# Kernel optimization log

Hardware: AMD Instinct MI355X
Metric: run time of the kernel (lower is better)

The kernel has to match this reference:

```python
import jax, jax.numpy as jnp
import numpy as np


def setup_inputs() -> dict:
    key = jax.random.key(0)
    B, F, H, W, C_out = 8, 64, 128, 128, 32
    V = H * W                     # grid vertices
    E = 3 * V                     # edges; flattened connectivity has 6V entries -> degree 6
    F2 = F // 2
    dim_channel = 6 * F2          # 192
    mid = dim_channel // 2        # 96
    out_ch = 2 * C_out            # 64
    k1, k2, k3, k4 = jax.random.split(key, 4)
    features = jax.random.normal(k1, (B, F, E), dtype=jnp.float32)
    # each vertex appears exactly 6 times in the flattened connectivity
    conn_flat = jax.random.permutation(k2, jnp.tile(jnp.arange(V, dtype=jnp.int32), 6))
    connectivity = conn_flat.reshape(E, 2)
    W1 = jax.random.normal(k3, (dim_channel, mid), dtype=jnp.float32) / np.sqrt(dim_channel)
    b1 = jnp.zeros((mid,), dtype=jnp.float32)
    W2 = jax.random.normal(k4, (mid, out_ch), dtype=jnp.float32) / np.sqrt(mid)
    b2 = jnp.zeros((out_ch,), dtype=jnp.float32)
    return {"features": features, "connectivity": connectivity,
            "output_dim": (H, W, C_out), "W1": W1, "b1": b1, "W2": W2, "b2": b2}


def _occurrence_rank(edges):
    # occ[i] = number of j < i with edges[j] == edges[i] (matches the serial
    # images_index bookkeeping in the torch loop). Stable argsort groups equal
    # vertices while preserving original order within a group.
    n = edges.shape[0]
    order = jnp.argsort(edges)            # stable by default in jax
    sorted_e = edges[order]
    first = jnp.searchsorted(sorted_e, sorted_e, side='left')
    rank_sorted = (jnp.arange(n) - first).astype(jnp.int32)
    return jnp.zeros(n, dtype=jnp.int32).at[order].set(rank_sorted)


def reference(features, connectivity, output_dim, W1, b1, W2, b2):
    B, F, E = features.shape
    H, Wd, C_out = int(output_dim[0]), int(output_dim[1]), int(output_dim[2])
    V = H * Wd
    F2 = F // 2
    edges = connectivity.reshape(-1)                      # [2E]
    # [B, F, E] -> [B, E, F] -> [B, 2E, F/2]: one half-feature per edge endpoint
    mesh = jnp.transpose(features, (0, 2, 1)).reshape(B, 2 * E, F2)
    occ = _occurrence_rank(edges)                         # slot per endpoint, 0..5
    # scatter half-features into [B, V, 6, F/2]; (vertex, slot) pairs are unique
    img = jnp.zeros((B, V, 6, F2), features.dtype).at[:, edges, occ, :].set(mesh)
    x = img.reshape(B, H, Wd, 6 * F2).transpose(0, 3, 1, 2)   # [B, 6*F/2, H, W]
    # 1x1 ConvTranspose2d == pointwise GEMM (torch weight layout [in, out, 1, 1])
    y = jax.nn.relu(jnp.einsum('bihw,io->bohw', x, W1) + b1[None, :, None, None])
    out = jax.nn.relu(jnp.einsum('bihw,io->bohw', y, W2) + b2[None, :, None, None])
    return out
```

## Files before the change

kernel.cpp:

```cpp
#include <hip/hip_runtime.h>
#include <hip/hip_bf16.h>
#include <stdint.h>

namespace {
constexpr int Bb   = 8;
constexpr int Ff   = 64;
constexpr int Ee   = 49152;
constexpr int Vv   = 16384;
constexpr int F2   = 32;
constexpr int TWOE = 2 * Ee;
constexpr int MID  = 96;
constexpr int OUTC = 64;
constexpr int DIMC = 192;
}

typedef __attribute__((ext_vector_type(8))) short bf16x8;
typedef __attribute__((ext_vector_type(4))) float f32x4;

__global__ void zero_cnt(int* __restrict__ cnt) {
    int i = blockIdx.x * 256 + threadIdx.x;
    if (i < Vv) cnt[i] = 0;
}

__global__ void bucket_fill(const int* __restrict__ conn, int* __restrict__ cnt,
                            int* __restrict__ buckets) {
    int i = blockIdx.x * 256 + threadIdx.x;
    if (i >= TWOE) return;
    int v = conn[i];
    int pos = atomicAdd(&cnt[v], 1);
    if (pos < 6) buckets[v * 6 + pos] = i;
}

__global__ void sort6(int* __restrict__ buckets) {
    int v = blockIdx.x * 256 + threadIdx.x;
    if (v >= Vv) return;
    int a[6];
#pragma unroll
    for (int k = 0; k < 6; ++k) a[k] = buckets[v * 6 + k];
#define CSWAP(x, y) { int lo = min(a[x], a[y]); int hi = max(a[x], a[y]); a[x] = lo; a[y] = hi; }
    CSWAP(1, 2) CSWAP(4, 5) CSWAP(0, 2) CSWAP(3, 5) CSWAP(0, 1) CSWAP(3, 4)
    CSWAP(2, 5) CSWAP(0, 3) CSWAP(1, 4) CSWAP(2, 4) CSWAP(1, 3) CSWAP(2, 3)
#undef CSWAP
#pragma unroll
    for (int k = 0; k < 6; ++k) buckets[v * 6 + k] = a[k];
}

__global__ __launch_bounds__(256) void transpose_feats(const float* __restrict__ feat,
                                                       __hip_bfloat16* __restrict__ meshT) {
    __shared__ float tile[64][65];
    const int b  = blockIdx.y;
    const int e0 = blockIdx.x * 64;
    const int t  = threadIdx.x;
    const float* src = feat + (size_t)b * Ff * Ee;
#pragma unroll
    for (int k = 0; k < 16; ++k) {
        int idx = k * 256 + t;
        int c = idx >> 6;
        int e = idx & 63;
        tile[c][e] = src[(size_t)c * Ee + e0 + e];
    }
    __syncthreads();
    __hip_bfloat16* dst = meshT + (size_t)b * ((size_t)Ee * 64) + (size_t)e0 * 64;
#pragma unroll
    for (int k = 0; k < 16; ++k) {
        int idx = k * 256 + t;
        int e = idx >> 6;
        int c = idx & 63;
        dst[e * 64 + c] = __float2bfloat16(tile[c][e]);
    }
}

__global__ void prep_weights(const float* __restrict__ W1, const float* __restrict__ W2,
                             __hip_bfloat16* __restrict__ w1f, __hip_bfloat16* __restrict__ w2f) {
    int tid = blockIdx.x * 256 + threadIdx.x;
    if (tid < 18432) {
        int j = tid & 7, l = (tid >> 3) & 63, ft = tid >> 9;
        int kk = ft / 6, nt = ft - kk * 6;
        int k = kk * 32 + (l >> 4) * 8 + j;
        int n = nt * 16 + (l & 15);
        w1f[tid] = __float2bfloat16(W1[k * MID + n]);
    } else if (tid < 24576) {
        int t2 = tid - 18432;
        int j = t2 & 7, l = (t2 >> 3) & 63, ft = t2 >> 9;
        int kk = ft >> 2, nt = ft & 3;
        int k = kk * 32 + (l >> 4) * 8 + j;
        int n = nt * 16 + (l & 15);
        w2f[t2] = __float2bfloat16(W2[k * OUTC + n]);
    }
}

__global__ __launch_bounds__(256, 4) void fused_mfma(
    const __hip_bfloat16* __restrict__ meshT,
    const int* __restrict__ perm,
    const __hip_bfloat16* __restrict__ w1f, const float* __restrict__ b1,
    const __hip_bfloat16* __restrict__ w2f, const float* __restrict__ b2,
    float* __restrict__ out)
{
    __shared__ __align__(16) __hip_bfloat16 xs[64][200];
    __shared__ __align__(16) __hip_bfloat16 ys[64][104];
    const int t   = threadIdx.x;
    const int l   = t & 63;
    const int wid = t >> 6;
    const int b   = blockIdx.y;
    const int v0  = blockIdx.x * 64 + wid * 16;
    const int lr  = l & 15;
    const int lg  = l >> 4;

    const ushort* mbase = (const ushort*)meshT + (size_t)b * ((size_t)TWOE * F2);
#pragma unroll
    for (int it = 0; it < 6; ++it) {
        int flat = it * 64 + l;
        int vl = flat / 24;
        int r  = flat - vl * 24;
        int s  = r >> 2, c = r & 3;
        int i  = perm[(v0 + vl) * 6 + s];
        uint4 d = *reinterpret_cast<const uint4*>(mbase + (size_t)i * F2 + c * 8);
        *reinterpret_cast<uint4*>(&xs[wid * 16 + vl][s * 32 + c * 8]) = d;
    }
    __syncthreads();

    f32x4 acc[6];
#pragma unroll
    for (int nt = 0; nt < 6; ++nt) {
        float bv = b1[nt * 16 + lr];
        acc[nt] = (f32x4){bv, bv, bv, bv};
    }
#pragma unroll
    for (int kk = 0; kk < 6; ++kk) {
        bf16x8 a = *reinterpret_cast<const bf16x8*>(&xs[wid * 16 + lr][kk * 32 + lg * 8]);
#pragma unroll
        for (int nt = 0; nt < 6; ++nt) {
            bf16x8 w = *reinterpret_cast<const bf16x8*>(w1f + ((size_t)((kk * 6 + nt) * 64 + l) * 8));
            acc[nt] = __builtin_amdgcn_mfma_f32_16x16x32_bf16(a, w, acc[nt], 0, 0, 0);
        }
    }
#pragma unroll
    for (int nt = 0; nt < 6; ++nt) {
#pragma unroll
        for (int r = 0; r < 4; ++r) {
            ys[wid * 16 + lg * 4 + r][nt * 16 + lr] = __float2bfloat16(fmaxf(acc[nt][r], 0.0f));
        }
    }
    __syncthreads();

    f32x4 acc2[4];
#pragma unroll
    for (int nt = 0; nt < 4; ++nt) {
        float bv = b2[nt * 16 + lr];
        acc2[nt] = (f32x4){bv, bv, bv, bv};
    }
#pragma unroll
    for (int kk = 0; kk < 3; ++kk) {
        bf16x8 a = *reinterpret_cast<const bf16x8*>(&ys[wid * 16 + lr][kk * 32 + lg * 8]);
#pragma unroll
        for (int nt = 0; nt < 4; ++nt) {
            bf16x8 w = *reinterpret_cast<const bf16x8*>(w2f + ((size_t)((kk * 4 + nt) * 64 + l) * 8));
            acc2[nt] = __builtin_amdgcn_mfma_f32_16x16x32_bf16(a, w, acc2[nt], 0, 0, 0);
        }
    }

    const int vbase = v0 + lg * 4;
#pragma unroll
    for (int nt = 0; nt < 4; ++nt) {
        f32x4 o4;
#pragma unroll
        for (int r = 0; r < 4; ++r) o4[r] = fmaxf(acc2[nt][r], 0.0f);
        *reinterpret_cast<f32x4*>(out + (((size_t)(b * OUTC + nt * 16 + lr)) << 14) + vbase) = o4;
    }
}

extern "C" void kernel_launch(void* const* d_in, const int* in_sizes, int n_in,
                              void* d_out, int out_size, void* d_ws, size_t ws_size,
                              hipStream_t stream) {
    const float* feat = (const float*)d_in[0];
    const int*   conn = (const int*)d_in[1];
    const float* W1   = (const float*)d_in[3];
    const float* b1   = (const float*)d_in[4];
    const float* W2   = (const float*)d_in[5];
    const float* b2   = (const float*)d_in[6];
    float* out = (float*)d_out;

    char* ws = (char*)d_ws;
    int* cnt  = (int*)ws;
    int* perm = (int*)(ws + (size_t)Vv * 4);
    __hip_bfloat16* meshT = (__hip_bfloat16*)(ws + (size_t)Vv * 4 + (size_t)TWOE * 4);
    size_t meshT_bytes = (size_t)Bb * TWOE * F2 * 2;
    __hip_bfloat16* w1f = (__hip_bfloat16*)((char*)meshT + meshT_bytes);
    __hip_bfloat16* w2f = w1f + 18432;

    zero_cnt<<<(Vv + 255) / 256, 256, 0, stream>>>(cnt);
    bucket_fill<<<(TWOE + 255) / 256, 256, 0, stream>>>(conn, cnt, perm);
    sort6<<<(Vv + 255) / 256, 256, 0, stream>>>(perm);
    prep_weights<<<96, 256, 0, stream>>>(W1, W2, w1f, w2f);
    transpose_feats<<<dim3(Ee / 64, Bb), 256, 0, stream>>>(feat, meshT);
    fused_mfma<<<dim3(Vv / 64, Bb), 256, 0, stream>>>(meshT, perm, w1f, b1, w2f, b2, out);
}
```

Measured before the change: 72.01 us.

## Scatter features to vertex-major layout in transpose; read directly in MFMA kernel

Instead of gathering edge features through a sorted permutation inside the GEMM kernel, the permutation is inverted once into a destination map. The transpose kernel then scatters bf16 half-features directly into a vertex-major [B,V,192] buffer. The GEMM kernel reads A fragments straight from global memory, with no shared-memory staging and no barrier. This removes the indirect gather and one LDS round trip. In exchange the transpose does scattered 16-byte writes and the GEMM issues uncoalesced per-row global loads.

Result: faster. 67.50 us (-6.3%).

```diff
diff --git a/kernel.cpp b/kernel.cpp
--- a/kernel.cpp
+++ b/kernel.cpp
@@ -11,7 +11,6 @@
 constexpr int TWOE = 2 * Ee;
 constexpr int MID  = 96;
 constexpr int OUTC = 64;
-constexpr int DIMC = 192;
 }
 
 typedef __attribute__((ext_vector_type(8))) short bf16x8;
@@ -31,7 +30,7 @@
     if (pos < 6) buckets[v * 6 + pos] = i;
 }
 
-__global__ void sort6(int* __restrict__ buckets) {
+__global__ void sort6_inv(const int* __restrict__ buckets, int* __restrict__ dest) {
     int v = blockIdx.x * 256 + threadIdx.x;
     if (v >= Vv) return;
     int a[6];
@@ -42,32 +41,7 @@
     CSWAP(2, 5) CSWAP(0, 3) CSWAP(1, 4) CSWAP(2, 4) CSWAP(1, 3) CSWAP(2, 3)
 #undef CSWAP
 #pragma unroll
-    for (int k = 0; k < 6; ++k) buckets[v * 6 + k] = a[k];
-}
-
-__global__ __launch_bounds__(256) void transpose_feats(const float* __restrict__ feat,
-                                                       __hip_bfloat16* __restrict__ meshT) {
-    __shared__ float tile[64][65];
-    const int b  = blockIdx.y;
-    const int e0 = blockIdx.x * 64;
-    const int t  = threadIdx.x;
-    const float* src = feat + (size_t)b * Ff * Ee;
-#pragma unroll
-    for (int k = 0; k < 16; ++k) {
-        int idx = k * 256 + t;
-        int c = idx >> 6;
-        int e = idx & 63;
-        tile[c][e] = src[(size_t)c * Ee + e0 + e];
-    }
-    __syncthreads();
-    __hip_bfloat16* dst = meshT + (size_t)b * ((size_t)Ee * 64) + (size_t)e0 * 64;
-#pragma unroll
-    for (int k = 0; k < 16; ++k) {
-        int idx = k * 256 + t;
-        int e = idx >> 6;
-        int c = idx & 63;
-        dst[e * 64 + c] = __float2bfloat16(tile[c][e]);
-    }
+    for (int k = 0; k < 6; ++k) dest[a[k]] = v * 6 + k;
 }
 
 __global__ void prep_weights(const float* __restrict__ W1, const float* __restrict__ W2,
@@ -89,14 +63,47 @@
     }
 }
 
-__global__ __launch_bounds__(256, 4) void fused_mfma(
-    const __hip_bfloat16* __restrict__ meshT,
-    const int* __restrict__ perm,
+__global__ __launch_bounds__(256) void scatter_feats(const float* __restrict__ feat,
+                                                     const int* __restrict__ dest,
+                                                     ushort* __restrict__ xg) {
+    __shared__ float tile[64][65];
+    const int b  = blockIdx.y;
+    const int e0 = blockIdx.x * 64;
+    const int t  = threadIdx.x;
+    const float* src = feat + (size_t)b * Ff * Ee;
+#pragma unroll
+    for (int k = 0; k < 16; ++k) {
+        int idx = k * 256 + t;
+        int c = idx >> 6;
+        int e = idx & 63;
+        tile[c][e] = src[(size_t)c * Ee + e0 + e];
+    }
+    __syncthreads();
+    ushort* dst_base = xg + (size_t)b * ((size_t)Vv * 192);
+#pragma unroll
+    for (int it = 0; it < 2; ++it) {
+        int item = it * 256 + t;
+        int le = item >> 2, s2 = item & 3;
+        int e = le >> 1, h = le & 1;
+        int i = e0 * 2 + e * 2 + h;
+        int d = dest[i];
+        int c0 = h * 32 + s2 * 8;
+        union { ushort u[8]; uint4 q; } pk;
+#pragma unroll
+        for (int k = 0; k < 8; ++k) {
+            __hip_bfloat16 hv = __float2bfloat16(tile[c0 + k][e]);
+            pk.u[k] = *reinterpret_cast<ushort*>(&hv);
+        }
+        *reinterpret_cast<uint4*>(dst_base + (size_t)d * 32 + s2 * 8) = pk.q;
+    }
+}
+
+__global__ __launch_bounds__(256) void decode_mfma(
+    const ushort* __restrict__ xg,
     const __hip_bfloat16* __restrict__ w1f, const float* __restrict__ b1,
     const __hip_bfloat16* __restrict__ w2f, const float* __restrict__ b2,
     float* __restrict__ out)
 {
-    __shared__ __align__(16) __hip_bfloat16 xs[64][200];
     __shared__ __align__(16) __hip_bfloat16 ys[64][104];
     const int t   = threadIdx.x;
     const int l   = t & 63;
@@ -106,18 +113,7 @@
     const int lr  = l & 15;
     const int lg  = l >> 4;
 
-    const ushort* mbase = (const ushort*)meshT + (size_t)b * ((size_t)TWOE * F2);
-#pragma unroll
-    for (int it = 0; it < 6; ++it) {
-        int flat = it * 64 + l;
-        int vl = flat / 24;
-        int r  = flat - vl * 24;
-        int s  = r >> 2, c = r & 3;
-        int i  = perm[(v0 + vl) * 6 + s];
-        uint4 d = *reinterpret_cast<const uint4*>(mbase + (size_t)i * F2 + c * 8);
-        *reinterpret_cast<uint4*>(&xs[wid * 16 + vl][s * 32 + c * 8]) = d;
-    }
-    __syncthreads();
+    const ushort* xv = xg + ((size_t)b * Vv + v0) * 192;
 
     f32x4 acc[6];
 #pragma unroll
@@ -127,7 +123,7 @@
     }
 #pragma unroll
     for (int kk = 0; kk < 6; ++kk) {
-        bf16x8 a = *reinterpret_cast<const bf16x8*>(&xs[wid * 16 + lr][kk * 32 + lg * 8]);
+        bf16x8 a = *reinterpret_cast<const bf16x8*>(xv + (size_t)lr * 192 + kk * 32 + lg * 8);
 #pragma unroll
         for (int nt = 0; nt < 6; ++nt) {
             bf16x8 w = *reinterpret_cast<const bf16x8*>(w1f + ((size_t)((kk * 6 + nt) * 64 + l) * 8));
@@ -181,17 +177,17 @@
     float* out = (float*)d_out;
 
     char* ws = (char*)d_ws;
-    int* cnt  = (int*)ws;
-    int* perm = (int*)(ws + (size_t)Vv * 4);
-    __hip_bfloat16* meshT = (__hip_bfloat16*)(ws + (size_t)Vv * 4 + (size_t)TWOE * 4);
-    size_t meshT_bytes = (size_t)Bb * TWOE * F2 * 2;
-    __hip_bfloat16* w1f = (__hip_bfloat16*)((char*)meshT + meshT_bytes);
+    int* cnt     = (int*)ws;
+    int* buckets = (int*)(ws + 65536);
+    int* dest    = (int*)(ws + 65536 + 393216);
+    __hip_bfloat16* w1f = (__hip_bfloat16*)(ws + 65536 + 2 * 393216);
     __hip_bfloat16* w2f = w1f + 18432;
+    ushort* xg = (ushort*)(ws + 65536 + 2 * 393216 + 49152);
 
     zero_cnt<<<(Vv + 255) / 256, 256, 0, stream>>>(cnt);
-    bucket_fill<<<(TWOE + 255) / 256, 256, 0, stream>>>(conn, cnt, perm);
-    sort6<<<(Vv + 255) / 256, 256, 0, stream>>>(perm);
+    bucket_fill<<<(TWOE + 255) / 256, 256, 0, stream>>>(conn, cnt, buckets);
+    sort6_inv<<<(Vv + 255) / 256, 256, 0, stream>>>(buckets, dest);
     prep_weights<<<96, 256, 0, stream>>>(W1, W2, w1f, w2f);
-    transpose_feats<<<dim3(Ee / 64, Bb), 256, 0, stream>>>(feat, meshT);
-    fused_mfma<<<dim3(Vv / 64, Bb), 256, 0, stream>>>(meshT, perm, w1f, b1, w2f, b2, out);
+    scatter_feats<<<dim3(Ee / 64, Bb), 256, 0, stream>>>(feat, dest, xg);
+    decode_mfma<<<dim3(Vv / 64, Bb), 256, 0, stream>>>(xg, w1f, b1, w2f, b2, out);
 }
```
